# Optimization experiments

Hardware: AMD Instinct MI355X
Metric: run time of the kernel (lower is better)

Reference implementation:

```python
import jax, jax.numpy as jnp
import numpy as np

K = 3      # fixed 3x3 kernel in module
PAD = 1    # padding=1, stride=1, dilation=1, groups=1, deformable_groups=1


def _conv2d(x, w, b=None, pad=PAD):
    out = jax.lax.conv_general_dilated(
        x, w, window_strides=(1, 1), padding=((pad, pad), (pad, pad)),
        dimension_numbers=('NCHW', 'OIHW', 'NCHW'))
    if b is not None:
        out = out + b[None, :, None, None]
    return out


def _bilinear_gather(x, py, px):
    # x: [B,C,H,W]; py,px: [B,KK,H,W] float sampling coords (zero-pad outside)
    B, C, H, W = x.shape
    y0 = jnp.floor(py)
    x0 = jnp.floor(px)
    wy1 = py - y0
    wx1 = px - x0
    wy0 = 1.0 - wy1
    wx0 = 1.0 - wx1
    y0i = y0.astype(jnp.int32)
    x0i = x0.astype(jnp.int32)
    xf = x.reshape(B, C, H * W)

    def corner(yi, xi, w):
        valid = (yi >= 0) & (yi < H) & (xi >= 0) & (xi < W)
        yc = jnp.clip(yi, 0, H - 1)
        xc = jnp.clip(xi, 0, W - 1)
        idx = (yc * W + xc).reshape(B, -1)                     # [B, KK*H*W]
        v = jnp.take_along_axis(xf, idx[:, None, :], axis=2)  # [B, C, KK*H*W]
        return v * (w * valid).reshape(B, 1, -1)

    out = (corner(y0i,     x0i,     wy0 * wx0)
         + corner(y0i,     x0i + 1, wy0 * wx1)
         + corner(y0i + 1, x0i,     wy1 * wx0)
         + corner(y0i + 1, x0i + 1, wy1 * wx1))
    KK = py.shape[1]
    return out.reshape(B, C, KK, H, W)


def _deform_forward(x, offset_w, offset_b, conv_w):
    B, C, H, W = x.shape
    # offset branch: plain 3x3 conv -> [B, 2*K*K, H, W], layout (k, (dy,dx))
    off = _conv2d(x, offset_w, offset_b).reshape(B, K * K, 2, H, W)
    ys = jnp.arange(H, dtype=x.dtype)
    xs = jnp.arange(W, dtype=x.dtype)
    ky, kx = jnp.meshgrid(jnp.arange(K), jnp.arange(K), indexing='ij')
    ky = ky.reshape(-1).astype(x.dtype)   # [9]
    kx = kx.reshape(-1).astype(x.dtype)
    # sampling coords p = p0 + p_k + offset   -> [B, 9, H, W]
    py = ys[None, None, :, None] - PAD + ky[None, :, None, None] + off[:, :, 0]
    px = xs[None, None, None, :] - PAD + kx[None, :, None, None] + off[:, :, 1]
    sampled = _bilinear_gather(x, py, px)                       # [B,C,9,H,W]
    O = conv_w.shape[0]
    return jnp.einsum('bckhw,ock->bohw', sampled, conv_w.reshape(O, C, K * K))


def setup_inputs() -> dict:
    key = jax.random.key(0)
    k1, k2, k3 = jax.random.split(key, 3)
    B, C, O, H, W = 8, 256, 256, 64, 64
    x = jax.random.normal(k1, (B, C, H, W), dtype=jnp.float32)
    # small random offset weights so learned offsets are ~ +/- 2 px
    offset_w = jax.random.normal(k2, (2 * K * K, C, K, K), dtype=jnp.float32) * 0.05
    offset_b = jnp.zeros((2 * K * K,), dtype=jnp.float32)
    conv_w = jax.random.normal(k3, (O, C, K, K), dtype=jnp.float32) * 0.02
    return {"x": x, "offset_w": offset_w, "offset_b": offset_b, "conv_w": conv_w}


def reference(x, offset_w, offset_b, conv_w):
    return _deform_forward(x, offset_w, offset_b, conv_w)
```

## Files before the change

kernel.cpp:

```cpp
#include <hip/hip_runtime.h>

using short8 = __attribute__((ext_vector_type(8))) short;
using f32x4  = __attribute__((ext_vector_type(4))) float;

__device__ inline unsigned short f2bf(float f) {
  unsigned u = __float_as_uint(f);
  u += 0x7fffu + ((u >> 16) & 1u);
  return (unsigned short)(u >> 16);
}
__device__ inline float bf2f(short s) {
  return __uint_as_float(((unsigned)(unsigned short)s) << 16);
}

__device__ inline void barrier_lgkm() {
  asm volatile("s_waitcnt lgkmcnt(0)\n\ts_barrier" ::: "memory");
}

__global__ __launch_bounds__(256) void prep_xT(const float* __restrict__ x,
                                               unsigned short* __restrict__ xT,
                                               unsigned short* __restrict__ xTlo) {
  __shared__ float tile[32 * 268];
  int bid = blockIdx.x;
  int xh = bid & 1, y = (bid >> 1) & 63, b = bid >> 7;
  int tid = threadIdx.x;
  int xc = tid & 31, cq = tid >> 5;
#pragma unroll 4
  for (int i = 0; i < 32; ++i) {
    int c = i * 8 + cq;
    tile[xc * 268 + c] =
        x[(((size_t)((b << 8) + c)) << 12) + (y << 6) + xh * 32 + xc];
  }
  __syncthreads();
#pragma unroll 2
  for (int i = 0; i < 8; ++i) {
    int u = i * 256 + tid;
    int site = u >> 6, c4 = u & 63;
    float4 v = *(const float4*)(tile + site * 268 + c4 * 4);
    ushort4 hi, lo;
    hi.x = f2bf(v.x); lo.x = f2bf(v.x - bf2f(hi.x));
    hi.y = f2bf(v.y); lo.y = f2bf(v.y - bf2f(hi.y));
    hi.z = f2bf(v.z); lo.z = f2bf(v.z - bf2f(hi.z));
    hi.w = f2bf(v.w); lo.w = f2bf(v.w - bf2f(hi.w));
    size_t addr = (((size_t)((b << 12) + (y << 6) + xh * 32 + site)) << 8) + c4 * 4;
    *(ushort4*)(xT + addr) = hi;
    *(ushort4*)(xTlo + addr) = lo;
  }
}

__global__ void prep_w_all(const float* __restrict__ cw, const float* __restrict__ ow,
                           unsigned short* __restrict__ wBt2,
                           unsigned short* __restrict__ wOt,
                           unsigned short* __restrict__ wOtLo) {
  int bid = blockIdx.x;
  if (bid < 2304) {
    int e = bid * 256 + threadIdx.x;
    int kc = e & 31, o = (e >> 5) & 255, ks = e >> 13;
    int c = (ks & 7) * 32 + kc, kt = ks >> 3;
    wBt2[e] = f2bf(cw[(size_t)(o * 256 + c) * 9 + kt]);
  } else {
    int e = (bid - 2304) * 256 + threadIdx.x;
    int kc = e & 31, o = (e >> 5) & 31, ks = e >> 10;
    int c = (ks & 7) * 32 + kc, kt = ks >> 3;
    float v = (o < 18) ? ow[(size_t)(o * 256 + c) * 9 + kt] : 0.f;
    unsigned short hi = f2bf(v);
    wOt[e] = hi;
    wOtLo[e] = f2bf(v - bf2f(hi));
  }
}

__device__ inline void gatherOff2(const unsigned short* xT, const unsigned short* xTlo,
                                  const unsigned short* zp, int b, int h, int p16,
                                  int q, int ccg, int ky, int kx,
                                  short8* gh, short8* gl) {
  int y = h + ky - 1;
  bool yv = (unsigned)y < 64u;
  int yc = min(max(y, 0), 63);
#pragma unroll
  for (int i = 0; i < 4; ++i) {
    int px = i * 16 + p16;
    int xx = px + kx - 1;
    bool v = yv && ((unsigned)xx < 64u);
    int xc = min(max(xx, 0), 63);
    size_t base = (((size_t)((b << 12) + (yc << 6) + xc)) << 8) + ccg * 32 + q * 8;
    const unsigned short* ph = v ? (xT + base) : zp;
    const unsigned short* pl = v ? (xTlo + base) : zp;
    gh[i] = *(const short8*)ph;
    gl[i] = *(const short8*)pl;
  }
}
__device__ inline void loadBOff2(const unsigned short* wOt, const unsigned short* wOtLo,
                                 int ks, int m16, int quad, short8* bh, short8* bl) {
  const unsigned short* bp = wOt + (ks << 10) + m16 * 32 + quad * 8;
  const unsigned short* bq = wOtLo + (ks << 10) + m16 * 32 + quad * 8;
  bh[0] = *(const short8*)bp;  bh[1] = *(const short8*)(bp + 512);
  bl[0] = *(const short8*)bq;  bl[1] = *(const short8*)(bq + 512);
}

__global__ __launch_bounds__(64) void offset_conv2(
    const unsigned short* __restrict__ xT, const unsigned short* __restrict__ xTlo,
    const unsigned short* __restrict__ wOt, const unsigned short* __restrict__ wOtLo,
    const unsigned short* __restrict__ zp, float* out) {
  __shared__ unsigned short Ah[2 * 2560], Al[2 * 2560];
  int lane = threadIdx.x;
  int bid = blockIdx.x;
  int b = bid & 7, h = (bid >> 3) & 63, half = bid >> 9;
  int m16 = lane & 15, quad = lane >> 4;
  int p16 = lane >> 2, q = lane & 3;
  int cc0 = half * 4;
  f32x4 acc[4][2];
#pragma unroll
  for (int mt = 0; mt < 4; ++mt)
#pragma unroll
    for (int j = 0; j < 2; ++j) acc[mt][j] = (f32x4){0.f, 0.f, 0.f, 0.f};

  short8 gh[4], gl[4], bh[2], bl[2];
  gatherOff2(xT, xTlo, zp, b, h, p16, q, cc0, 0, 0, gh, gl);
  loadBOff2(wOt, wOtLo, cc0, m16, quad, bh, bl);

  for (int it = 0; it < 36; ++it) {
    int buf = it & 1;
#pragma unroll
    for (int i = 0; i < 4; ++i) {
      int px = i * 16 + p16;
      *(short8*)(Ah + buf * 2560 + px * 40 + q * 8) = gh[i];
      *(short8*)(Al + buf * 2560 + px * 40 + q * 8) = gl[i];
    }
    int jn = it + 1;
    int ccn = cc0 + jn / 9, r9 = jn % 9;
    int kyn = r9 / 3, kxn = r9 - kyn * 3;
    short8 ghn[4], gln[4], bhn[2], bln[2];
    loadBOff2(wOt, wOtLo, (kyn * 3 + kxn) * 8 + ccn, m16, quad, bhn, bln);
    gatherOff2(xT, xTlo, zp, b, h, p16, q, ccn, kyn, kxn, ghn, gln);
#pragma unroll
    for (int mt = 0; mt < 4; ++mt) {
      short8 ah = *(const short8*)(Ah + buf * 2560 + (mt * 16 + m16) * 40 + quad * 8);
      short8 al = *(const short8*)(Al + buf * 2560 + (mt * 16 + m16) * 40 + quad * 8);
#pragma unroll
      for (int j = 0; j < 2; ++j) {
        acc[mt][j] = __builtin_amdgcn_mfma_f32_16x16x32_bf16(ah, bh[j], acc[mt][j], 0, 0, 0);
        acc[mt][j] = __builtin_amdgcn_mfma_f32_16x16x32_bf16(al, bh[j], acc[mt][j], 0, 0, 0);
        acc[mt][j] = __builtin_amdgcn_mfma_f32_16x16x32_bf16(ah, bl[j], acc[mt][j], 0, 0, 0);
      }
    }
#pragma unroll
    for (int i = 0; i < 4; ++i) { gh[i] = ghn[i]; gl[i] = gln[i]; }
    bh[0] = bhn[0]; bh[1] = bhn[1]; bl[0] = bln[0]; bl[1] = bln[1];
  }
#pragma unroll
  for (int j = 0; j < 2; ++j) {
    int o = j * 16 + m16;
    if (o < 18) {
      float* po = out + (((size_t)((b << 8) + 200 + half * 18 + o)) << 12) + (h << 6);
#pragma unroll
      for (int mt = 0; mt < 4; ++mt)
#pragma unroll
        for (int rr = 0; rr < 4; ++rr)
          po[mt * 16 + quad * 4 + rr] = acc[mt][j][rr];
    }
  }
}

__device__ inline void gather4(const unsigned short* __restrict__ xT,
                               int bbase, int q, int jt,
                               const int2* cif2, const float4* cwf4,
                               int px, short8* g, float4& wq) {
  int cc = jt / 9, kt = jt - cc * 9;
  int2 si = cif2[kt * 64 + px];
  wq = cwf4[kt * 64 + px];
  const unsigned short* base = xT + (size_t)(unsigned)(bbase + cc * 32 + q * 8);
  g[0] = *(const short8*)(base + si.x);
  g[1] = *(const short8*)(base + si.x + 256);
  g[2] = *(const short8*)(base + si.y);
  g[3] = *(const short8*)(base + si.y + 256);
}
__device__ inline void loadB(const unsigned short* __restrict__ wBt2, int wave,
                             int m16, int quad, int jt, short8* bf) {
  int cc = jt / 9, kt = jt - cc * 9;
  int ks = kt * 8 + cc;
  const unsigned short* bp =
      wBt2 + ((size_t)ks << 13) + (wave << 11) + m16 * 32 + quad * 8;
#pragma unroll
  for (int j = 0; j < 4; ++j)
    bf[j] = *(const short8*)(bp + j * 512);
}

__global__ __launch_bounds__(256, 2) void deform_main(
    const unsigned short* __restrict__ xT, const float* __restrict__ offb,
    const unsigned short* __restrict__ wBt2, float* out) {
  __shared__ float4 smem4[2080];
  char* smem = (char*)smem4;
  float4* cwf4 = (float4*)smem;
  int2*   cif2 = (int2*)(smem + 9216);
  unsigned short* At = (unsigned short*)(smem + 13824);

  int tid = threadIdx.x, lane = tid & 63, wave = tid >> 6;
  int b = blockIdx.x & 7, h = blockIdx.x >> 3;

  size_t bb = ((size_t)(b << 8)) << 12;
  for (int it = tid; it < 576; it += 256) {
    int k = it >> 6, px = it & 63;
    int ky = k / 3, kx = k - ky * 3;
    int idx = (h << 6) + px;
    float dy = out[bb + (((size_t)(200 + 2 * k)) << 12) + idx] +
               out[bb + (((size_t)(218 + 2 * k)) << 12) + idx] + offb[2 * k];
    float dx = out[bb + (((size_t)(201 + 2 * k)) << 12) + idx] +
               out[bb + (((size_t)(219 + 2 * k)) << 12) + idx] + offb[2 * k + 1];
    float py = (float)(h - 1 + ky) + dy;
    float pxx = (float)(px - 1 + kx) + dx;
    float y0f = floorf(py), x0f = floorf(pxx);
    int y0 = (int)y0f, x0 = (int)x0f;
    float wy1 = py - y0f, wx1 = pxx - x0f;
    int xb; float wxl, wxr;
    if (x0 >= 0 && x0 <= 62)      { xb = x0; wxl = 1.f - wx1; wxr = wx1; }
    else if (x0 == -1)            { xb = 0;  wxl = wx1;       wxr = 0.f; }
    else if (x0 == 63)            { xb = 62; wxl = 0.f;       wxr = 1.f - wx1; }
    else                          { xb = 0;  wxl = 0.f;       wxr = 0.f; }
    float wy0v = ((unsigned)y0 < 64u) ? (1.f - wy1) : 0.f;
    float wy1v = ((unsigned)(y0 + 1) < 64u) ? wy1 : 0.f;
    int yc0 = min(max(y0, 0), 63), yc1 = min(max(y0 + 1, 0), 63);
    cwf4[it] = make_float4(wy0v * wxl, wy0v * wxr, wy1v * wxl, wy1v * wxr);
    cif2[it] = make_int2(((yc0 << 6) + xb) << 8, ((yc1 << 6) + xb) << 8);
  }
  __syncthreads();

  int m16 = lane & 15, quad = lane >> 4;
  int px = wave * 16 + (lane >> 2);
  int q  = lane & 3;
  int bbase = b << 20;
  f32x4 acc[4][4];
#pragma unroll
  for (int i = 0; i < 4; ++i)
#pragma unroll
    for (int j = 0; j < 4; ++j) acc[i][j] = (f32x4){0.f, 0.f, 0.f, 0.f};

  short8 g[4]; float4 wq; short8 bcur[4];
  gather4(xT, bbase, q, 0, cif2, cwf4, px, g, wq);
  loadB(wBt2, wave, m16, quad, 0, bcur);

  for (int it = 0; it < 72; ++it) {
    int buf = it & 1;
    short8 av;
#pragma unroll
    for (int i = 0; i < 8; ++i) {
      float v = wq.x * bf2f(g[0][i]) + wq.y * bf2f(g[1][i]) +
                wq.z * bf2f(g[2][i]) + wq.w * bf2f(g[3][i]);
      av[i] = (short)f2bf(v);
    }
    *(short8*)(At + buf * 2560 + px * 40 + q * 8) = av;
    int jn = (it < 71) ? it + 1 : 71;
    short8 bnext[4], gn[4]; float4 wqn;
    loadB(wBt2, wave, m16, quad, jn, bnext);
    gather4(xT, bbase, q, jn, cif2, cwf4, px, gn, wqn);
    barrier_lgkm();
    short8 af[4];
#pragma unroll
    for (int mt = 0; mt < 4; ++mt)
      af[mt] = *(const short8*)(At + buf * 2560 + (mt * 16 + m16) * 40 + quad * 8);
#pragma unroll
    for (int mt = 0; mt < 4; ++mt)
#pragma unroll
      for (int j = 0; j < 4; ++j)
        acc[mt][j] = __builtin_amdgcn_mfma_f32_16x16x32_bf16(af[mt], bcur[j],
                                                             acc[mt][j], 0, 0, 0);
#pragma unroll
    for (int i = 0; i < 4; ++i) g[i] = gn[i];
    wq = wqn;
#pragma unroll
    for (int j = 0; j < 4; ++j) bcur[j] = bnext[j];
  }
  __syncthreads();

  float* ep = (float*)smem;
  for (int half = 0; half < 2; ++half) {
    if ((wave >> 1) == half) {
#pragma unroll
      for (int mt = 0; mt < 4; ++mt)
#pragma unroll
        for (int j = 0; j < 4; ++j)
#pragma unroll
          for (int rr = 0; rr < 4; ++rr) {
            int o_loc = (wave & 1) * 64 + j * 16 + m16;
            int ppx = mt * 16 + quad * 4 + rr;
            ep[o_loc * 65 + ppx] = acc[mt][j][rr];
          }
    }
    __syncthreads();
#pragma unroll 4
    for (int t = 0; t < 32; ++t) {
      int idx = t * 256 + tid;
      int o = idx >> 6, ppx = idx & 63;
      out[(((size_t)((b << 8) + half * 128 + o)) << 12) + (h << 6) + ppx] =
          ep[o * 65 + ppx];
    }
    __syncthreads();
  }
}

extern "C" void kernel_launch(void* const* d_in, const int* in_sizes, int n_in,
                              void* d_out, int out_size, void* d_ws, size_t ws_size,
                              hipStream_t stream) {
  const float* x     = (const float*)d_in[0];
  const float* offw  = (const float*)d_in[1];
  const float* offb  = (const float*)d_in[2];
  const float* convw = (const float*)d_in[3];
  float* out = (float*)d_out;

  char* ws = (char*)d_ws;
  unsigned short* wOt   = (unsigned short*)ws;
  unsigned short* wOtLo = (unsigned short*)(ws + 147456);
  unsigned short* wBt2  = (unsigned short*)(ws + 294912);
  unsigned short* xT    = (unsigned short*)(ws + 1474560);
  unsigned short* xTlo  = (unsigned short*)(ws + 18251776);
  const unsigned short* zp = wOt + 768;

  prep_xT<<<1024, 256, 0, stream>>>(x, xT, xTlo);
  prep_w_all<<<2592, 256, 0, stream>>>(convw, offw, wBt2, wOt, wOtLo);
  offset_conv2<<<1024, 64, 0, stream>>>(xT, xTlo, wOt, wOtLo, zp, out);
  deform_main<<<512, 256, 0, stream>>>(xT, offb, wBt2, out);
}
```

Before: 192.6 us.

## Split offset conv over 8 channel chunks, merge prep kernels, drop LDS epilogue

Merges the two prep kernels into one launch. Splits the offset convolution into 8 channel-chunk partials (4096 one-wave blocks instead of 1024), so each block runs 9 iterations instead of 36. The partials are stored in the output scratch area and summed by deform_main. The main kernel's epilogue now writes float4 straight from the accumulators instead of staging through shared memory, which also shrinks LDS use. The cost is more partial-sum traffic: 8 reads per offset value instead of 2.

```diff
diff --git a/kernel.cpp b/kernel.cpp
--- a/kernel.cpp
+++ b/kernel.cpp
@@ -16,49 +16,44 @@
   asm volatile("s_waitcnt lgkmcnt(0)\n\ts_barrier" ::: "memory");
 }
 
-__global__ __launch_bounds__(256) void prep_xT(const float* __restrict__ x,
-                                               unsigned short* __restrict__ xT,
-                                               unsigned short* __restrict__ xTlo) {
+__global__ __launch_bounds__(256) void prep_all(
+    const float* __restrict__ x, const float* __restrict__ cw,
+    const float* __restrict__ ow, unsigned short* __restrict__ xT,
+    unsigned short* __restrict__ xTlo, unsigned short* __restrict__ wBt2,
+    unsigned short* __restrict__ wOt, unsigned short* __restrict__ wOtLo) {
   __shared__ float tile[32 * 268];
-  int bid = blockIdx.x;
-  int xh = bid & 1, y = (bid >> 1) & 63, b = bid >> 7;
-  int tid = threadIdx.x;
-  int xc = tid & 31, cq = tid >> 5;
+  int bid = blockIdx.x, tid = threadIdx.x;
+  if (bid < 1024) {
+    int xh = bid & 1, y = (bid >> 1) & 63, b = bid >> 7;
+    int xc = tid & 31, cq = tid >> 5;
 #pragma unroll 4
-  for (int i = 0; i < 32; ++i) {
-    int c = i * 8 + cq;
-    tile[xc * 268 + c] =
-        x[(((size_t)((b << 8) + c)) << 12) + (y << 6) + xh * 32 + xc];
-  }
-  __syncthreads();
+    for (int i = 0; i < 32; ++i) {
+      int c = i * 8 + cq;
+      tile[xc * 268 + c] =
+          x[(((size_t)((b << 8) + c)) << 12) + (y << 6) + xh * 32 + xc];
+    }
+    __syncthreads();
 #pragma unroll 2
-  for (int i = 0; i < 8; ++i) {
-    int u = i * 256 + tid;
-    int site = u >> 6, c4 = u & 63;
-    float4 v = *(const float4*)(tile + site * 268 + c4 * 4);
-    ushort4 hi, lo;
-    hi.x = f2bf(v.x); lo.x = f2bf(v.x - bf2f(hi.x));
-    hi.y = f2bf(v.y); lo.y = f2bf(v.y - bf2f(hi.y));
-    hi.z = f2bf(v.z); lo.z = f2bf(v.z - bf2f(hi.z));
-    hi.w = f2bf(v.w); lo.w = f2bf(v.w - bf2f(hi.w));
-    size_t addr = (((size_t)((b << 12) + (y << 6) + xh * 32 + site)) << 8) + c4 * 4;
-    *(ushort4*)(xT + addr) = hi;
-    *(ushort4*)(xTlo + addr) = lo;
-  }
-}
-
-__global__ void prep_w_all(const float* __restrict__ cw, const float* __restrict__ ow,
-                           unsigned short* __restrict__ wBt2,
-                           unsigned short* __restrict__ wOt,
-                           unsigned short* __restrict__ wOtLo) {
-  int bid = blockIdx.x;
-  if (bid < 2304) {
-    int e = bid * 256 + threadIdx.x;
+    for (int i = 0; i < 8; ++i) {
+      int u = i * 256 + tid;
+      int site = u >> 6, c4 = u & 63;
+      float4 v = *(const float4*)(tile + site * 268 + c4 * 4);
+      ushort4 hi, lo;
+      hi.x = f2bf(v.x); lo.x = f2bf(v.x - bf2f(hi.x));
+      hi.y = f2bf(v.y); lo.y = f2bf(v.y - bf2f(hi.y));
+      hi.z = f2bf(v.z); lo.z = f2bf(v.z - bf2f(hi.z));
+      hi.w = f2bf(v.w); lo.w = f2bf(v.w - bf2f(hi.w));
+      size_t addr = (((size_t)((b << 12) + (y << 6) + xh * 32 + site)) << 8) + c4 * 4;
+      *(ushort4*)(xT + addr) = hi;
+      *(ushort4*)(xTlo + addr) = lo;
+    }
+  } else if (bid < 3328) {
+    int e = (bid - 1024) * 256 + tid;
     int kc = e & 31, o = (e >> 5) & 255, ks = e >> 13;
     int c = (ks & 7) * 32 + kc, kt = ks >> 3;
     wBt2[e] = f2bf(cw[(size_t)(o * 256 + c) * 9 + kt]);
   } else {
-    int e = (bid - 2304) * 256 + threadIdx.x;
+    int e = (bid - 3328) * 256 + tid;
     int kc = e & 31, o = (e >> 5) & 31, ks = e >> 10;
     int c = (ks & 7) * 32 + kc, kt = ks >> 3;
     float v = (o < 18) ? ow[(size_t)(o * 256 + c) * 9 + kt] : 0.f;
@@ -96,17 +91,16 @@
   bl[0] = *(const short8*)bq;  bl[1] = *(const short8*)(bq + 512);
 }
 
-__global__ __launch_bounds__(64) void offset_conv2(
+__global__ __launch_bounds__(64) void offset_conv3(
     const unsigned short* __restrict__ xT, const unsigned short* __restrict__ xTlo,
     const unsigned short* __restrict__ wOt, const unsigned short* __restrict__ wOtLo,
     const unsigned short* __restrict__ zp, float* out) {
   __shared__ unsigned short Ah[2 * 2560], Al[2 * 2560];
   int lane = threadIdx.x;
   int bid = blockIdx.x;
-  int b = bid & 7, h = (bid >> 3) & 63, half = bid >> 9;
+  int b = bid & 7, h = (bid >> 3) & 63, ccq = bid >> 9;
   int m16 = lane & 15, quad = lane >> 4;
   int p16 = lane >> 2, q = lane & 3;
-  int cc0 = half * 4;
   f32x4 acc[4][2];
 #pragma unroll
   for (int mt = 0; mt < 4; ++mt)
@@ -114,10 +108,10 @@
     for (int j = 0; j < 2; ++j) acc[mt][j] = (f32x4){0.f, 0.f, 0.f, 0.f};
 
   short8 gh[4], gl[4], bh[2], bl[2];
-  gatherOff2(xT, xTlo, zp, b, h, p16, q, cc0, 0, 0, gh, gl);
-  loadBOff2(wOt, wOtLo, cc0, m16, quad, bh, bl);
-
-  for (int it = 0; it < 36; ++it) {
+  gatherOff2(xT, xTlo, zp, b, h, p16, q, ccq, 0, 0, gh, gl);
+  loadBOff2(wOt, wOtLo, ccq, m16, quad, bh, bl);
+
+  for (int it = 0; it < 9; ++it) {
     int buf = it & 1;
 #pragma unroll
     for (int i = 0; i < 4; ++i) {
@@ -125,12 +119,11 @@
       *(short8*)(Ah + buf * 2560 + px * 40 + q * 8) = gh[i];
       *(short8*)(Al + buf * 2560 + px * 40 + q * 8) = gl[i];
     }
-    int jn = it + 1;
-    int ccn = cc0 + jn / 9, r9 = jn % 9;
-    int kyn = r9 / 3, kxn = r9 - kyn * 3;
+    int jn = (it < 8) ? it + 1 : 8;
+    int kyn = jn / 3, kxn = jn - kyn * 3;
     short8 ghn[4], gln[4], bhn[2], bln[2];
-    loadBOff2(wOt, wOtLo, (kyn * 3 + kxn) * 8 + ccn, m16, quad, bhn, bln);
-    gatherOff2(xT, xTlo, zp, b, h, p16, q, ccn, kyn, kxn, ghn, gln);
+    loadBOff2(wOt, wOtLo, jn * 8 + ccq, m16, quad, bhn, bln);
+    gatherOff2(xT, xTlo, zp, b, h, p16, q, ccq, kyn, kxn, ghn, gln);
 #pragma unroll
     for (int mt = 0; mt < 4; ++mt) {
       short8 ah = *(const short8*)(Ah + buf * 2560 + (mt * 16 + m16) * 40 + quad * 8);
@@ -150,7 +143,7 @@
   for (int j = 0; j < 2; ++j) {
     int o = j * 16 + m16;
     if (o < 18) {
-      float* po = out + (((size_t)((b << 8) + 200 + half * 18 + o)) << 12) + (h << 6);
+      float* po = out + (((size_t)((b << 8) + 100 + ccq * 18 + o)) << 12) + (h << 6);
 #pragma unroll
       for (int mt = 0; mt < 4; ++mt)
 #pragma unroll
@@ -187,7 +180,7 @@
 __global__ __launch_bounds__(256, 2) void deform_main(
     const unsigned short* __restrict__ xT, const float* __restrict__ offb,
     const unsigned short* __restrict__ wBt2, float* out) {
-  __shared__ float4 smem4[2080];
+  __shared__ float4 smem4[1504];
   char* smem = (char*)smem4;
   float4* cwf4 = (float4*)smem;
   int2*   cif2 = (int2*)(smem + 9216);
@@ -201,10 +194,12 @@
     int k = it >> 6, px = it & 63;
     int ky = k / 3, kx = k - ky * 3;
     int idx = (h << 6) + px;
-    float dy = out[bb + (((size_t)(200 + 2 * k)) << 12) + idx] +
-               out[bb + (((size_t)(218 + 2 * k)) << 12) + idx] + offb[2 * k];
-    float dx = out[bb + (((size_t)(201 + 2 * k)) << 12) + idx] +
-               out[bb + (((size_t)(219 + 2 * k)) << 12) + idx] + offb[2 * k + 1];
+    float dy = offb[2 * k], dx = offb[2 * k + 1];
+#pragma unroll
+    for (int qq = 0; qq < 8; ++qq) {
+      dy += out[bb + (((size_t)(100 + qq * 18 + 2 * k)) << 12) + idx];
+      dx += out[bb + (((size_t)(101 + qq * 18 + 2 * k)) << 12) + idx];
+    }
     float py = (float)(h - 1 + ky) + dy;
     float pxx = (float)(px - 1 + kx) + dx;
     float y0f = floorf(py), x0f = floorf(pxx);
@@ -268,31 +263,17 @@
 #pragma unroll
     for (int j = 0; j < 4; ++j) bcur[j] = bnext[j];
   }
-  __syncthreads();
-
-  float* ep = (float*)smem;
-  for (int half = 0; half < 2; ++half) {
-    if ((wave >> 1) == half) {
-#pragma unroll
-      for (int mt = 0; mt < 4; ++mt)
-#pragma unroll
-        for (int j = 0; j < 4; ++j)
-#pragma unroll
-          for (int rr = 0; rr < 4; ++rr) {
-            int o_loc = (wave & 1) * 64 + j * 16 + m16;
-            int ppx = mt * 16 + quad * 4 + rr;
-            ep[o_loc * 65 + ppx] = acc[mt][j][rr];
-          }
-    }
-    __syncthreads();
-#pragma unroll 4
-    for (int t = 0; t < 32; ++t) {
-      int idx = t * 256 + tid;
-      int o = idx >> 6, ppx = idx & 63;
-      out[(((size_t)((b << 8) + half * 128 + o)) << 12) + (h << 6) + ppx] =
-          ep[o * 65 + ppx];
-    }
-    __syncthreads();
+
+#pragma unroll
+  for (int j = 0; j < 4; ++j) {
+    int o = wave * 64 + j * 16 + m16;
+    float* po = out + (((size_t)((b << 8) + o)) << 12) + (h << 6) + quad * 4;
+#pragma unroll
+    for (int mt = 0; mt < 4; ++mt) {
+      float4 v = make_float4(acc[mt][j][0], acc[mt][j][1], acc[mt][j][2],
+                             acc[mt][j][3]);
+      *(float4*)(po + mt * 16) = v;
+    }
   }
 }
 
@@ -313,8 +294,7 @@
   unsigned short* xTlo  = (unsigned short*)(ws + 18251776);
   const unsigned short* zp = wOt + 768;
 
-  prep_xT<<<1024, 256, 0, stream>>>(x, xT, xTlo);
-  prep_w_all<<<2592, 256, 0, stream>>>(convw, offw, wBt2, wOt, wOtLo);
-  offset_conv2<<<1024, 64, 0, stream>>>(xT, xTlo, wOt, wOtLo, zp, out);
+  prep_all<<<3616, 256, 0, stream>>>(x, convw, offw, xT, xTlo, wBt2, wOt, wOtLo);
+  offset_conv3<<<4096, 64, 0, stream>>>(xT, xTlo, wOt, wOtLo, zp, out);
   deform_main<<<512, 256, 0, stream>>>(xT, offb, wBt2, out);
 }
```

Result: faster. 185.0 us (-3.9%).
